# Kernel optimization log

Hardware: AMD Instinct MI355X
Metric: run time of the kernel (lower is better)

The kernel has to match this reference:

```python
import jax, jax.numpy as jnp
from jax import lax
import numpy as np

EPS = 1e-06


def conv1x1(x, W, b):
    # x: [B,C,H,W], W: [O,C], b: [O]
    return jnp.einsum('bchw,oc->bohw', x, W) + b[None, :, None, None]


def conv3x3(x, W, b):
    # W: [O,I,3,3], 'SAME' padding
    y = lax.conv_general_dilated(x, W, (1, 1), 'SAME',
                                 dimension_numbers=('NCHW', 'OIHW', 'NCHW'))
    return y + b[None, :, None, None]


def setup_inputs() -> dict:
    key = jax.random.key(0)
    ks = jax.random.split(key, 13)
    B, C, H, W = 8, 64, 256, 256
    kc, vc = 64, 64
    s = 0.05
    return {
        'x':  jax.random.normal(ks[0], (B, C, H, W), jnp.float32),
        'Wq': jax.random.normal(ks[1], (kc, C), jnp.float32) * s,
        'bq': jax.random.normal(ks[2], (kc,), jnp.float32) * s,
        'Wk': jax.random.normal(ks[3], (kc, C), jnp.float32) * s,
        'bk': jax.random.normal(ks[4], (kc,), jnp.float32) * s,
        'Wv': jax.random.normal(ks[5], (vc, C), jnp.float32) * s,
        'bv': jax.random.normal(ks[6], (vc,), jnp.float32) * s,
        'Wr': jax.random.normal(ks[7], (C, vc), jnp.float32) * s,
        'br': jax.random.normal(ks[8], (C,), jnp.float32) * s,
        'W1': jax.random.normal(ks[9], (C, C, 3, 3), jnp.float32) * s,
        'b1': jax.random.normal(ks[10], (C,), jnp.float32) * s,
        'W2': jax.random.normal(ks[11], (C, C, 3, 3), jnp.float32) * s,
        'b2': jax.random.normal(ks[12], (C,), jnp.float32) * s,
    }


def reference(x, Wq, bq, Wk, bk, Wv, bv, Wr, br, W1, b1, W2, b2):
    B, C, H, W = x.shape
    N = H * W
    kc = Wq.shape[0]
    vc = Wv.shape[0]

    Q = conv1x1(x, Wq, bq).reshape(B, kc, N)
    K = conv1x1(x, Wk, bk).reshape(B, kc, N)
    V = conv1x1(x, Wv, bv).reshape(B, vc, N)

    # L2-normalize over the channel axis (dim=-2 in torch)
    Qn = Q / jnp.linalg.norm(Q, axis=1, keepdims=True)   # [B,kc,N]
    Kn = K / jnp.linalg.norm(K, axis=1, keepdims=True)   # [B,kc,N]
    Qt = jnp.transpose(Qn, (0, 2, 1))                     # [B,N,kc]

    # denominator: 1 / (N + Q . (sum_n K + eps))
    k_sum = Kn.sum(axis=-1) + EPS                         # [B,kc]
    denom = 1.0 / (N + jnp.einsum('bnc,bc->bn', Qt, k_sum))  # [B,N]

    value_sum = V.sum(axis=-1, keepdims=True)             # [B,vc,1]

    # linear-attention aggregation: KV^T then Q.(KV)
    agg_kv = jnp.einsum('bmn,bcn->bmc', Kn, V)            # [B,kc,vc]
    # the per-batch/per-head torch loop sums head slices of the full kc
    # contraction -> equivalent to a single einsum over kc
    agg_qkv = jnp.einsum('bmc,bnm->bcn', agg_kv, Qt)      # [B,vc,N]

    numerator = value_sum + agg_qkv                       # [B,vc,N]
    weight_value = (numerator * denom[:, None, :]).reshape(B, vc, H, W)

    attn = conv1x1(weight_value, Wr, br)                  # [B,C,H,W]
    out = conv3x3(conv3x3(attn, W1, b1), W2, b2) * x + x
    return out
```

## Files before the change

kernel.cpp:

```cpp
#include <hip/hip_runtime.h>

typedef __attribute__((ext_vector_type(8))) short short8;
typedef __attribute__((ext_vector_type(4))) float f32x4;
typedef __attribute__((ext_vector_type(4))) int i32x4;

#define NPIX 65536
#define KPITCH 264
#define RED_KSUM 0
#define RED_VSUM 512
#define RED_AGG 1024

__device__ __forceinline__ float b2f(unsigned short u) {
  union { unsigned int i; float f; } z; z.i = ((unsigned int)u) << 16; return z.f;
}
__device__ __forceinline__ unsigned short f2b(float f) {
  union { float f; unsigned int i; } z; z.f = f;
  unsigned int r = z.i + 0x7fffu + ((z.i >> 16) & 1u);
  return (unsigned short)(r >> 16);
}
__device__ __forceinline__ unsigned int packbf(float a, float b) {
  return (unsigned int)f2b(a) | ((unsigned int)f2b(b) << 16);
}
__device__ __forceinline__ int cvtpk(float a, float b) {
  int r;
  asm("v_cvt_pk_bf16_f32 %0, %1, %2" : "=v"(r) : "v"(a), "v"(b));
  return r;
}

__global__ __launch_bounds__(256) void prep_kernel(
    const float* __restrict__ W1, const float* __restrict__ W2,
    const float* __restrict__ Wq, const float* __restrict__ Wk,
    const float* __restrict__ Wv,
    unsigned short* __restrict__ wA, unsigned short* __restrict__ wQKV,
    float* __restrict__ red)
{
  const int i = blockIdx.x * 256 + threadIdx.x;
  if (i < 73728) {
    const float* W = (i < 36864) ? W1 : W2;
    const int e = (i < 36864) ? i : (i - 36864);
    const int j    = e & 7;
    const int lane = (e >> 3) & 63;
    const int mt   = (e >> 9) & 3;
    const int kb   = (e >> 11) & 1;
    const int tap  = e >> 12;
    const int o = mt * 16 + (lane & 15);
    const int c = kb * 32 + ((lane >> 4) << 3) + j;
    wA[i] = f2b(W[o * 576 + c * 9 + tap]);
  } else if (i < 86016) {
    const int e = i - 73728;
    const int j    = e & 7;
    const int lane = (e >> 3) & 63;
    const int mt   = (e >> 9) & 3;
    const int kb   = (e >> 11) & 1;
    const int pj   = e >> 12;
    const float* W = (pj == 0) ? Wq : (pj == 1) ? Wk : Wv;
    const int o = mt * 16 + (lane & 15);
    const int c = kb * 32 + ((lane >> 4) << 3) + j;
    wQKV[e] = f2b(W[o * 64 + c]);
  } else if (i < 119808) {
    red[i - 86016] = 0.0f;
  }
}

#define PROJ(PIDX, BM)                                                         \
    {                                                                          \
      _Pragma("unroll")                                                        \
      for (int mt = 0; mt < 4; ++mt) {                                         \
        const f32x4 bb = *(const f32x4*)((BM) + mt * 16 + g * 4);              \
        _Pragma("unroll")                                                      \
        for (int nt = 0; nt < 4; ++nt) acc[mt][nt] = bb;                       \
      }                                                                        \
      _Pragma("unroll")                                                        \
      for (int kb = 0; kb < 2; ++kb) {                                         \
        const unsigned short* wp = wQKV + ((PIDX) * 2 + kb) * 2048 + l * 8;    \
        short8 af[4];                                                          \
        _Pragma("unroll")                                                      \
        for (int mt = 0; mt < 4; ++mt)                                         \
          af[mt] = *(const short8*)(wp + mt * 512);                            \
        _Pragma("unroll")                                                      \
        for (int mt = 0; mt < 4; ++mt)                                         \
          _Pragma("unroll")                                                    \
          for (int nt = 0; nt < 4; ++nt)                                       \
            acc[mt][nt] = __builtin_amdgcn_mfma_f32_16x16x32_bf16(             \
                af[mt], bf[nt][kb], acc[mt][nt], 0, 0, 0);                     \
      }                                                                        \
    }

__global__ __launch_bounds__(256, 2) void qkv_kernel(
    const float* __restrict__ x,
    const unsigned short* __restrict__ wQKV,
    const float* __restrict__ bq, const float* __restrict__ bk,
    const float* __restrict__ bv,
    unsigned short* __restrict__ Qn, float* __restrict__ red)
{
  __shared__ __align__(16) unsigned short sh[2 * 64 * KPITCH];
  unsigned short* ks = sh;
  unsigned short* vs = sh + 64 * KPITCH;
  unsigned int* shu = (unsigned int*)sh;
  const int b = blockIdx.y;
  const int t = threadIdx.x;
  const int w = t >> 6;
  const int l = t & 63;
  const int g = l >> 4;
  const int l15 = l & 15;
  const size_t xb = (size_t)b * 64 * NPIX;

  const f32x4 zero = {0.f, 0.f, 0.f, 0.f};
  f32x4 agg[4]  = {zero, zero, zero, zero};
  f32x4 kacc[4] = {zero, zero, zero, zero};
  f32x4 vacc[4] = {zero, zero, zero, zero};

  for (int it = 0; it < 4; ++it) {
    const int pxw = (blockIdx.x << 10) + (it << 8) + (w << 6);

    short8 bf[4][2];
#pragma unroll
    for (int nt = 0; nt < 4; ++nt) {
      const float* xp = x + xb + (size_t)(g * 8) * NPIX + pxw + nt * 16 + l15;
#pragma unroll
      for (int kb = 0; kb < 2; ++kb) {
        float f[8];
#pragma unroll
        for (int j = 0; j < 8; ++j)
          f[j] = xp[(size_t)(kb * 32 + j) * NPIX];
        union { i32x4 i; short8 s; } u;
        u.i.x = cvtpk(f[0], f[1]); u.i.y = cvtpk(f[2], f[3]);
        u.i.z = cvtpk(f[4], f[5]); u.i.w = cvtpk(f[6], f[7]);
        bf[nt][kb] = u.s;
      }
    }

    f32x4 acc[4][4];

    PROJ(0, bq);
    {
      float rq[4];
#pragma unroll
      for (int nt = 0; nt < 4; ++nt) {
        float ss = 0.f;
#pragma unroll
        for (int mt = 0; mt < 4; ++mt)
#pragma unroll
          for (int r = 0; r < 4; ++r)
            ss = fmaf(acc[mt][nt][r], acc[mt][nt][r], ss);
        ss += __shfl_xor(ss, 16);
        ss += __shfl_xor(ss, 32);
        rq[nt] = rsqrtf(ss);
      }
      unsigned int* sw = shu + w * 2304;
#pragma unroll
      for (int mt = 0; mt < 4; ++mt)
#pragma unroll
        for (int nt = 0; nt < 4; ++nt) {
          const int px = nt * 16 + l15;
          unsigned int* dst = sw + px * 36 + mt * 8 + g * 2;
          dst[0] = (unsigned)cvtpk(acc[mt][nt][0] * rq[nt], acc[mt][nt][1] * rq[nt]);
          dst[1] = (unsigned)cvtpk(acc[mt][nt][2] * rq[nt], acc[mt][nt][3] * rq[nt]);
        }
      const uint4* rr4 = (const uint4*)(shu + w * 2304);
#pragma unroll
      for (int k8 = 0; k8 < 8; ++k8) {
        const int p = (k8 << 3) + (l >> 3);
        const int ch8 = l & 7;
        *(uint4*)(Qn + ((size_t)b * NPIX + pxw + p) * 64 + ch8 * 8) =
            rr4[p * 9 + ch8];
      }
      __syncthreads();
    }

    PROJ(1, bk);
    {
      float rk[4];
#pragma unroll
      for (int nt = 0; nt < 4; ++nt) {
        float ss = 0.f;
#pragma unroll
        for (int mt = 0; mt < 4; ++mt)
#pragma unroll
          for (int r = 0; r < 4; ++r)
            ss = fmaf(acc[mt][nt][r], acc[mt][nt][r], ss);
        ss += __shfl_xor(ss, 16);
        ss += __shfl_xor(ss, 32);
        rk[nt] = rsqrtf(ss);
      }
#pragma unroll
      for (int mt = 0; mt < 4; ++mt)
#pragma unroll
        for (int nt = 0; nt < 4; ++nt)
#pragma unroll
          for (int r = 0; r < 4; ++r) {
            const float kn = acc[mt][nt][r] * rk[nt];
            kacc[mt][r] += kn;
            ks[(mt * 16 + g * 4 + r) * KPITCH + (w << 6) + nt * 16 + l15] =
                (unsigned short)cvtpk(kn, 0.f);
          }
    }

    PROJ(2, bv);
    {
#pragma unroll
      for (int mt = 0; mt < 4; ++mt)
#pragma unroll
        for (int nt = 0; nt < 4; ++nt)
#pragma unroll
          for (int r = 0; r < 4; ++r) {
            const float vv = acc[mt][nt][r];
            vacc[mt][r] += vv;
            vs[(mt * 16 + g * 4 + r) * KPITCH + (w << 6) + nt * 16 + l15] =
                (unsigned short)cvtpk(vv, 0.f);
          }
    }
    __syncthreads();

#pragma unroll
    for (int s = 0; s < 8; ++s) {
      const short8 ak =
          *(const short8*)(ks + (w * 16 + l15) * KPITCH + s * 32 + g * 8);
#pragma unroll
      for (int nt = 0; nt < 4; ++nt) {
        const short8 bv8 =
            *(const short8*)(vs + (nt * 16 + l15) * KPITCH + s * 32 + g * 8);
        agg[nt] = __builtin_amdgcn_mfma_f32_16x16x32_bf16(ak, bv8, agg[nt], 0, 0, 0);
      }
    }
    __syncthreads();
  }

#pragma unroll
  for (int mt = 0; mt < 4; ++mt)
#pragma unroll
    for (int r = 0; r < 4; ++r) {
      float kv = kacc[mt][r], vv = vacc[mt][r];
#pragma unroll
      for (int d = 1; d < 16; d <<= 1) {
        kv += __shfl_xor(kv, d);
        vv += __shfl_xor(vv, d);
      }
      if (l15 == 0) {
        atomicAdd(red + RED_KSUM + b * 64 + mt * 16 + g * 4 + r, kv);
        atomicAdd(red + RED_VSUM + b * 64 + mt * 16 + g * 4 + r, vv);
      }
    }
  float* ab = red + RED_AGG + b * 4096;
#pragma unroll
  for (int nt = 0; nt < 4; ++nt)
#pragma unroll
    for (int r = 0; r < 4; ++r)
      atomicAdd(ab + (w * 16 + g * 4 + r) * 64 + nt * 16 + l15, agg[nt][r]);
}

__global__ __launch_bounds__(256) void prep2_kernel(
    const float* __restrict__ Wr, const float* __restrict__ red,
    unsigned short* __restrict__ Cb, float* __restrict__ u,
    float* __restrict__ ks2)
{
  const int b = blockIdx.y;
  const int t = threadIdx.x;
  const int o = t & 63;
  const int kq = t >> 6;
  const float* wr = Wr + o * 64;
  const float* agg = red + RED_AGG + b * 4096;
#pragma unroll
  for (int i = 0; i < 4; ++i) {
    const int k = blockIdx.x * 16 + kq * 4 + i;
    const float* ar = agg + k * 64;
    float s = 0.f;
#pragma unroll
    for (int v = 0; v < 64; ++v) s = fmaf(wr[v], ar[v], s);
    const int mt = o >> 4, kb = k >> 5;
    const int lane = (o & 15) | (((k >> 3) & 3) << 4);
    const int j = k & 7;
    const unsigned short c1 = f2b(s);
    const float r1 = s - b2f(c1);
    Cb[b * 4096 + ((kb * 4 + mt) * 64 + lane) * 8 + j] = c1;
    Cb[32768 + b * 4096 + ((kb * 4 + mt) * 64 + lane) * 8 + j] = f2b(r1);
  }
  if (blockIdx.x == 0 && t < 64) {
    const float* vsr = red + RED_VSUM + b * 64;
    float s = 0.f;
#pragma unroll
    for (int v = 0; v < 64; ++v) s = fmaf(Wr[t * 64 + v], vsr[v], s);
    u[b * 64 + t] = s;
    ks2[b * 64 + t] = red[RED_KSUM + b * 64 + t] + 1e-6f;
  }
}

__global__ __launch_bounds__(256, 2) void attn_kernel(
    const unsigned short* __restrict__ Qn,
    const unsigned short* __restrict__ Cb,
    const float* __restrict__ u,
    const float* __restrict__ ks2,
    const float* __restrict__ br,
    unsigned short* __restrict__ attn)
{
  __shared__ __align__(16) unsigned short att[256 * 72];
  const int b = blockIdx.y;
  const int t = threadIdx.x;
  const int w = t >> 6, l = t & 63, g = l >> 4, l15 = l & 15;

  short8 af[2][2][4];
#pragma unroll
  for (int lvl = 0; lvl < 2; ++lvl)
#pragma unroll
    for (int kb = 0; kb < 2; ++kb)
#pragma unroll
      for (int mt = 0; mt < 4; ++mt)
        af[lvl][kb][mt] = *(const short8*)(
            Cb + lvl * 32768 + b * 4096 + ((kb * 4 + mt) * 64 + l) * 8);
  f32x4 uu[4], brf[4];
#pragma unroll
  for (int mt = 0; mt < 4; ++mt) {
    uu[mt]  = *(const f32x4*)(u + b * 64 + mt * 16 + g * 4);
    brf[mt] = *(const f32x4*)(br + mt * 16 + g * 4);
  }
  float ksl[16];
#pragma unroll
  for (int kb = 0; kb < 2; ++kb)
#pragma unroll
    for (int j = 0; j < 8; ++j)
      ksl[kb * 8 + j] = ks2[b * 64 + kb * 32 + g * 8 + j];

  for (int it = 0; it < 4; ++it) {
    const int pxw = (blockIdx.x << 10) + (it << 8) + (w << 6);
    short8 qf[4][2];
    float denom[4];
#pragma unroll
    for (int nt = 0; nt < 4; ++nt) {
      const unsigned short* qp =
          Qn + ((size_t)b * NPIX + pxw + nt * 16 + l15) * 64 + g * 8;
      qf[nt][0] = *(const short8*)qp;
      qf[nt][1] = *(const short8*)(qp + 32);
      float ss = 0.f;
#pragma unroll
      for (int kb = 0; kb < 2; ++kb)
#pragma unroll
        for (int j = 0; j < 8; ++j)
          ss = fmaf(b2f((unsigned short)qf[nt][kb][j]), ksl[kb * 8 + j], ss);
      ss += __shfl_xor(ss, 16);
      ss += __shfl_xor(ss, 32);
      denom[nt] = 1.0f / (65536.0f + ss);
    }
    f32x4 acc[4][4];
#pragma unroll
    for (int mt = 0; mt < 4; ++mt)
#pragma unroll
      for (int nt = 0; nt < 4; ++nt) acc[mt][nt] = uu[mt];
#pragma unroll
    for (int kb = 0; kb < 2; ++kb)
#pragma unroll
      for (int mt = 0; mt < 4; ++mt)
#pragma unroll
        for (int nt = 0; nt < 4; ++nt) {
          acc[mt][nt] = __builtin_amdgcn_mfma_f32_16x16x32_bf16(
              af[0][kb][mt], qf[nt][kb], acc[mt][nt], 0, 0, 0);
          acc[mt][nt] = __builtin_amdgcn_mfma_f32_16x16x32_bf16(
              af[1][kb][mt], qf[nt][kb], acc[mt][nt], 0, 0, 0);
        }
    unsigned int* sw = (unsigned int*)att + w * 2304;
#pragma unroll
    for (int mt = 0; mt < 4; ++mt)
#pragma unroll
      for (int nt = 0; nt < 4; ++nt) {
        const int px = nt * 16 + l15;
        unsigned int* dst = sw + px * 36 + mt * 8 + g * 2;
        dst[0] = (unsigned)cvtpk(fmaf(acc[mt][nt][0], denom[nt], brf[mt][0]),
                                 fmaf(acc[mt][nt][1], denom[nt], brf[mt][1]));
        dst[1] = (unsigned)cvtpk(fmaf(acc[mt][nt][2], denom[nt], brf[mt][2]),
                                 fmaf(acc[mt][nt][3], denom[nt], brf[mt][3]));
      }
    const uint4* rr4 = (const uint4*)att + w * 576;
#pragma unroll
    for (int k8 = 0; k8 < 8; ++k8) {
      const int p = (k8 << 3) + (l >> 3);
      const int ch8 = l & 7;
      *(uint4*)(attn + ((size_t)b * NPIX + pxw + p) * 64 + ch8 * 8) =
          rr4[p * 9 + ch8];
    }
  }
}

template <int EPI>
__global__ __launch_bounds__(256, 3) void conv3_kernel(
    const unsigned short* __restrict__ in,
    const unsigned short* __restrict__ wA,
    const float* __restrict__ bias,
    const float* __restrict__ xin,
    unsigned short* __restrict__ outh,
    float* __restrict__ outf)
{
  __shared__ __align__(16) unsigned short tile[10 * 34 * 72];
  const int bz = blockIdx.z;
  const int ty0 = blockIdx.y << 3;
  const int tx0 = blockIdx.x << 5;
  const int tid = threadIdx.x;
  const size_t nb = (size_t)bz * NPIX;

  for (int s = tid; s < 2720; s += 256) {
    const int g = s & 7;
    const int pix = s >> 3;
    const int xx = pix % 34;
    const int row = pix / 34;
    const int gx = tx0 + xx - 1;
    const int gy = ty0 + row - 1;
    uint4 v = {0u, 0u, 0u, 0u};
    if ((unsigned)gx < 256u && (unsigned)gy < 256u)
      v = *(const uint4*)(in + ((nb + (gy << 8) + gx) << 6) + (g << 3));
    *(uint4*)(tile + pix * 72 + (g << 3)) = v;
  }
  __syncthreads();

  const int w = tid >> 6, lane = tid & 63, q = lane >> 4, l = lane & 15;
  f32x4 acc[4][4];
  {
#pragma unroll
    for (int mt = 0; mt < 4; ++mt) {
      const f32x4 bb = *(const f32x4*)(bias + mt * 16 + q * 4);
#pragma unroll
      for (int nt = 0; nt < 4; ++nt) acc[mt][nt] = bb;
    }
  }
  const short8* tp = (const short8*)tile;
  for (int tap = 0; tap < 9; ++tap) {
    const int dy = tap / 3, dx = tap - dy * 3;
#pragma unroll
    for (int kb = 0; kb < 2; ++kb) {
      const unsigned short* wp = wA + (tap * 2 + kb) * 2048 + lane * 8;
      short8 af[4];
#pragma unroll
      for (int mt = 0; mt < 4; ++mt) af[mt] = *(const short8*)(wp + mt * 512);
      short8 bf[4];
#pragma unroll
      for (int nt = 0; nt < 4; ++nt) {
        const int yl = (w << 1) + (nt >> 1) + dy;
        const int xl = ((nt & 1) << 4) + l + dx;
        bf[nt] = tp[(yl * 34 + xl) * 9 + (kb << 2) + q];
      }
#pragma unroll
      for (int mt = 0; mt < 4; ++mt)
#pragma unroll
        for (int nt = 0; nt < 4; ++nt)
          acc[mt][nt] = __builtin_amdgcn_mfma_f32_16x16x32_bf16(
              af[mt], bf[nt], acc[mt][nt], 0, 0, 0);
    }
  }

  if (EPI == 0) {
    __syncthreads();
    unsigned int* wreg = (unsigned int*)tile + w * 2304;
#pragma unroll
    for (int mt = 0; mt < 4; ++mt)
#pragma unroll
      for (int nt = 0; nt < 4; ++nt) {
        const int p = ((nt >> 1) << 5) + ((nt & 1) << 4) + l;
        unsigned int* dst = wreg + p * 36 + (mt << 3) + (q << 1);
        dst[0] = packbf(acc[mt][nt][0], acc[mt][nt][1]);
        dst[1] = packbf(acc[mt][nt][2], acc[mt][nt][3]);
      }
    __syncthreads();
    const uint4* rreg = (const uint4*)tile + w * 576;
#pragma unroll
    for (int k = 0; k < 8; ++k) {
      const int p = (k << 3) + (lane >> 3);
      const int ch = lane & 7;
      const int gx = tx0 + (p & 31);
      const int gy = ty0 + (w << 1) + (p >> 5);
      *(uint4*)(outh + ((nb + (gy << 8) + gx) << 6) + (ch << 3)) =
          rreg[p * 9 + ch];
    }
  } else {
#pragma unroll
    for (int mt = 0; mt < 4; ++mt)
#pragma unroll
      for (int nt = 0; nt < 4; ++nt) {
        const int gx = tx0 + ((nt & 1) << 4) + l;
        const int gy = ty0 + (w << 1) + (nt >> 1);
#pragma unroll
        for (int r = 0; r < 4; ++r) {
          const int o = (mt << 4) + (q << 2) + r;
          const size_t idx = (((size_t)bz * 64 + o) << 16) + (gy << 8) + gx;
          const float xo = xin[idx];
          outf[idx] = fmaf(acc[mt][nt][r], xo, xo);
        }
      }
  }
}

extern "C" void kernel_launch(void* const* d_in, const int* in_sizes, int n_in,
                              void* d_out, int out_size, void* d_ws, size_t ws_size,
                              hipStream_t stream) {
  (void)in_sizes; (void)n_in; (void)out_size; (void)ws_size;
  const float* x  = (const float*)d_in[0];
  const float* Wq = (const float*)d_in[1];
  const float* bq = (const float*)d_in[2];
  const float* Wk = (const float*)d_in[3];
  const float* bk = (const float*)d_in[4];
  const float* Wv = (const float*)d_in[5];
  const float* bv = (const float*)d_in[6];
  const float* Wr = (const float*)d_in[7];
  const float* br = (const float*)d_in[8];
  const float* W1 = (const float*)d_in[9];
  const float* b1 = (const float*)d_in[10];
  const float* W2 = (const float*)d_in[11];
  const float* b2 = (const float*)d_in[12];

  unsigned short* wA1 = (unsigned short*)d_ws;
  unsigned short* wA2 = wA1 + 36864;
  float* red = (float*)((char*)d_ws + 147456);
  unsigned short* bufA = (unsigned short*)((char*)d_ws + 294912);
  unsigned short* wQKV = (unsigned short*)((char*)d_ws + 294912);
  unsigned short* Cb = (unsigned short*)((char*)d_ws + 294912);
  float* u_  = (float*)((char*)d_ws + 294912 + 131072);
  float* ks2 = (float*)((char*)d_ws + 294912 + 133120);
  unsigned short* bufB = (unsigned short*)d_out;
  unsigned short* bufQ = (unsigned short*)((char*)d_out + 67108864);

  prep_kernel<<<468, 256, 0, stream>>>(W1, W2, Wq, Wk, Wv, wA1, wQKV, red);
  qkv_kernel<<<dim3(64, 8), 256, 0, stream>>>(x, wQKV, bq, bk, bv, bufQ, red);
  prep2_kernel<<<dim3(4, 8), 256, 0, stream>>>(Wr, red, Cb, u_, ks2);
  attn_kernel<<<dim3(64, 8), 256, 0, stream>>>(bufQ, Cb, u_, ks2, br, bufB);
  conv3_kernel<0><<<dim3(8, 32, 8), 256, 0, stream>>>(
      bufB, wA1, b1, nullptr, bufA, nullptr);
  conv3_kernel<1><<<dim3(8, 32, 8), 256, 0, stream>>>(
      bufA, wA2, b2, x, nullptr, (float*)d_out);
}
```

Before: 562.3 us.

## Fuse the two 3x3 convolutions into one kernel with halo recompute in LDS

Replaces the two separate conv3x3 launches with one 512-thread kernel. Six waves compute the first convolution over the 10x34 halo region, reading the input directly from global memory. They store the bf16 result in shared memory, and all eight waves then compute the second convolution plus the x-residual epilogue. This removes the write and re-read of the full intermediate activation buffer and one kernel launch. The cost is roughly a third more first-convolution work for the halo, uncached repeated global loads per tap instead of LDS staging, and idle waves during stage one. The workspace layout is also reshuffled so the attention output lives in the workspace instead of the output buffer.

Result: no change. 561.2 us (-0.2%).

```diff
diff --git a/kernel.cpp b/kernel.cpp
--- a/kernel.cpp
+++ b/kernel.cpp
@@ -379,110 +379,128 @@
   }
 }
 
-template <int EPI>
-__global__ __launch_bounds__(256, 3) void conv3_kernel(
+__global__ __launch_bounds__(512, 2) void fused_conv_kernel(
     const unsigned short* __restrict__ in,
     const unsigned short* __restrict__ wA,
-    const float* __restrict__ bias,
+    const float* __restrict__ b1, const float* __restrict__ b2,
     const float* __restrict__ xin,
-    unsigned short* __restrict__ outh,
     float* __restrict__ outf)
 {
-  __shared__ __align__(16) unsigned short tile[10 * 34 * 72];
+  __shared__ __align__(16) unsigned short mid[340 * 72];
   const int bz = blockIdx.z;
   const int ty0 = blockIdx.y << 3;
   const int tx0 = blockIdx.x << 5;
   const int tid = threadIdx.x;
+  const int w = tid >> 6, lane = tid & 63, q = lane >> 4, l = lane & 15;
   const size_t nb = (size_t)bz * NPIX;
 
-  for (int s = tid; s < 2720; s += 256) {
-    const int g = s & 7;
-    const int pix = s >> 3;
-    const int xx = pix % 34;
-    const int row = pix / 34;
-    const int gx = tx0 + xx - 1;
-    const int gy = ty0 + row - 1;
-    uint4 v = {0u, 0u, 0u, 0u};
-    if ((unsigned)gx < 256u && (unsigned)gy < 256u)
-      v = *(const uint4*)(in + ((nb + (gy << 8) + gx) << 6) + (g << 3));
-    *(uint4*)(tile + pix * 72 + (g << 3)) = v;
+  if (w < 6) {
+    f32x4 acc[4][4];
+#pragma unroll
+    for (int mt = 0; mt < 4; ++mt) {
+      const f32x4 bb = *(const f32x4*)(b1 + mt * 16 + q * 4);
+#pragma unroll
+      for (int nt = 0; nt < 4; ++nt) acc[mt][nt] = bb;
+    }
+    int ylv[4], xlv[4];
+#pragma unroll
+    for (int nt = 0; nt < 4; ++nt) {
+      const int mp = w * 64 + nt * 16 + l;
+      const int mpc = mp < 340 ? mp : 339;
+      ylv[nt] = mpc / 34;
+      xlv[nt] = mpc - ylv[nt] * 34;
+    }
+    for (int tap = 0; tap < 9; ++tap) {
+      const int dy = tap / 3, dx = tap - dy * 3;
+#pragma unroll
+      for (int kb = 0; kb < 2; ++kb) {
+        const unsigned short* wp = wA + (tap * 2 + kb) * 2048 + lane * 8;
+        short8 af[4];
+#pragma unroll
+        for (int mt = 0; mt < 4; ++mt) af[mt] = *(const short8*)(wp + mt * 512);
+        short8 bfv[4];
+#pragma unroll
+        for (int nt = 0; nt < 4; ++nt) {
+          const int gy = ty0 + ylv[nt] + dy - 2;
+          const int gx = tx0 + xlv[nt] + dx - 2;
+          short8 v = {0, 0, 0, 0, 0, 0, 0, 0};
+          if ((unsigned)gy < 256u && (unsigned)gx < 256u)
+            v = *(const short8*)(
+                in + ((nb + (gy << 8) + gx) << 6) + ((kb * 4 + q) << 3));
+          bfv[nt] = v;
+        }
+#pragma unroll
+        for (int mt = 0; mt < 4; ++mt)
+#pragma unroll
+          for (int nt = 0; nt < 4; ++nt)
+            acc[mt][nt] = __builtin_amdgcn_mfma_f32_16x16x32_bf16(
+                af[mt], bfv[nt], acc[mt][nt], 0, 0, 0);
+      }
+    }
+    unsigned int* mu = (unsigned int*)mid;
+#pragma unroll
+    for (int nt = 0; nt < 4; ++nt) {
+      const int mp = w * 64 + nt * 16 + l;
+      if (mp < 340) {
+        const int gym = ty0 + ylv[nt] - 1;
+        const int gxm = tx0 + xlv[nt] - 1;
+        const bool ok = ((unsigned)gym < 256u) && ((unsigned)gxm < 256u);
+#pragma unroll
+        for (int mt = 0; mt < 4; ++mt) {
+          unsigned int* dst = mu + mp * 36 + mt * 8 + q * 2;
+          dst[0] = ok ? packbf(acc[mt][nt][0], acc[mt][nt][1]) : 0u;
+          dst[1] = ok ? packbf(acc[mt][nt][2], acc[mt][nt][3]) : 0u;
+        }
+      }
+    }
   }
   __syncthreads();
 
-  const int w = tid >> 6, lane = tid & 63, q = lane >> 4, l = lane & 15;
-  f32x4 acc[4][4];
-  {
-#pragma unroll
-    for (int mt = 0; mt < 4; ++mt) {
-      const f32x4 bb = *(const f32x4*)(bias + mt * 16 + q * 4);
-#pragma unroll
-      for (int nt = 0; nt < 4; ++nt) acc[mt][nt] = bb;
-    }
-  }
-  const short8* tp = (const short8*)tile;
+  f32x4 acc2[4][2];
+#pragma unroll
+  for (int mt = 0; mt < 4; ++mt) {
+    const f32x4 bb = *(const f32x4*)(b2 + mt * 16 + q * 4);
+    acc2[mt][0] = bb; acc2[mt][1] = bb;
+  }
+  const short8* tp2 = (const short8*)mid;
+  const unsigned short* wA2p = wA + 36864;
   for (int tap = 0; tap < 9; ++tap) {
     const int dy = tap / 3, dx = tap - dy * 3;
 #pragma unroll
     for (int kb = 0; kb < 2; ++kb) {
-      const unsigned short* wp = wA + (tap * 2 + kb) * 2048 + lane * 8;
+      const unsigned short* wp = wA2p + (tap * 2 + kb) * 2048 + lane * 8;
       short8 af[4];
 #pragma unroll
       for (int mt = 0; mt < 4; ++mt) af[mt] = *(const short8*)(wp + mt * 512);
-      short8 bf[4];
-#pragma unroll
-      for (int nt = 0; nt < 4; ++nt) {
-        const int yl = (w << 1) + (nt >> 1) + dy;
-        const int xl = ((nt & 1) << 4) + l + dx;
-        bf[nt] = tp[(yl * 34 + xl) * 9 + (kb << 2) + q];
+      short8 bf2[2];
+#pragma unroll
+      for (int nt = 0; nt < 2; ++nt) {
+        const int yl = w + dy;
+        const int xl = nt * 16 + l + dx;
+        bf2[nt] = tp2[(yl * 34 + xl) * 9 + (kb << 2) + q];
       }
 #pragma unroll
       for (int mt = 0; mt < 4; ++mt)
 #pragma unroll
-        for (int nt = 0; nt < 4; ++nt)
-          acc[mt][nt] = __builtin_amdgcn_mfma_f32_16x16x32_bf16(
-              af[mt], bf[nt], acc[mt][nt], 0, 0, 0);
-    }
-  }
-
-  if (EPI == 0) {
-    __syncthreads();
-    unsigned int* wreg = (unsigned int*)tile + w * 2304;
-#pragma unroll
-    for (int mt = 0; mt < 4; ++mt)
-#pragma unroll
-      for (int nt = 0; nt < 4; ++nt) {
-        const int p = ((nt >> 1) << 5) + ((nt & 1) << 4) + l;
-        unsigned int* dst = wreg + p * 36 + (mt << 3) + (q << 1);
-        dst[0] = packbf(acc[mt][nt][0], acc[mt][nt][1]);
-        dst[1] = packbf(acc[mt][nt][2], acc[mt][nt][3]);
-      }
-    __syncthreads();
-    const uint4* rreg = (const uint4*)tile + w * 576;
-#pragma unroll
-    for (int k = 0; k < 8; ++k) {
-      const int p = (k << 3) + (lane >> 3);
-      const int ch = lane & 7;
-      const int gx = tx0 + (p & 31);
-      const int gy = ty0 + (w << 1) + (p >> 5);
-      *(uint4*)(outh + ((nb + (gy << 8) + gx) << 6) + (ch << 3)) =
-          rreg[p * 9 + ch];
-    }
-  } else {
-#pragma unroll
-    for (int mt = 0; mt < 4; ++mt)
-#pragma unroll
-      for (int nt = 0; nt < 4; ++nt) {
-        const int gx = tx0 + ((nt & 1) << 4) + l;
-        const int gy = ty0 + (w << 1) + (nt >> 1);
-#pragma unroll
-        for (int r = 0; r < 4; ++r) {
-          const int o = (mt << 4) + (q << 2) + r;
-          const size_t idx = (((size_t)bz * 64 + o) << 16) + (gy << 8) + gx;
-          const float xo = xin[idx];
-          outf[idx] = fmaf(acc[mt][nt][r], xo, xo);
-        }
-      }
-  }
+        for (int nt = 0; nt < 2; ++nt)
+          acc2[mt][nt] = __builtin_amdgcn_mfma_f32_16x16x32_bf16(
+              af[mt], bf2[nt], acc2[mt][nt], 0, 0, 0);
+    }
+  }
+#pragma unroll
+  for (int mt = 0; mt < 4; ++mt)
+#pragma unroll
+    for (int nt = 0; nt < 2; ++nt) {
+      const int gx = tx0 + nt * 16 + l;
+      const int gy = ty0 + w;
+#pragma unroll
+      for (int r = 0; r < 4; ++r) {
+        const int o = (mt << 4) + (q << 2) + r;
+        const size_t idx = (((size_t)bz * 64 + o) << 16) + (gy << 8) + gx;
+        const float xo = xin[idx];
+        outf[idx] = fmaf(acc2[mt][nt][r], xo, xo);
+      }
+    }
 }
 
 extern "C" void kernel_launch(void* const* d_in, const int* in_sizes, int n_in,
@@ -503,23 +521,19 @@
   const float* W2 = (const float*)d_in[11];
   const float* b2 = (const float*)d_in[12];
 
-  unsigned short* wA1 = (unsigned short*)d_ws;
-  unsigned short* wA2 = wA1 + 36864;
-  float* red = (float*)((char*)d_ws + 147456);
-  unsigned short* bufA = (unsigned short*)((char*)d_ws + 294912);
-  unsigned short* wQKV = (unsigned short*)((char*)d_ws + 294912);
-  unsigned short* Cb = (unsigned short*)((char*)d_ws + 294912);
-  float* u_  = (float*)((char*)d_ws + 294912 + 131072);
-  float* ks2 = (float*)((char*)d_ws + 294912 + 133120);
-  unsigned short* bufB = (unsigned short*)d_out;
+  unsigned short* wA1  = (unsigned short*)d_ws;
+  unsigned short* wQKV = (unsigned short*)((char*)d_ws + 147456);
+  unsigned short* Cb   = (unsigned short*)((char*)d_ws + 147456);
+  float* u_  = (float*)((char*)d_ws + 278528);
+  float* ks2 = (float*)((char*)d_ws + 280576);
+  float* red = (float*)((char*)d_ws + 282624);
+  unsigned short* bufB = (unsigned short*)((char*)d_ws + 282624);
   unsigned short* bufQ = (unsigned short*)((char*)d_out + 67108864);
 
   prep_kernel<<<468, 256, 0, stream>>>(W1, W2, Wq, Wk, Wv, wA1, wQKV, red);
   qkv_kernel<<<dim3(64, 8), 256, 0, stream>>>(x, wQKV, bq, bk, bv, bufQ, red);
   prep2_kernel<<<dim3(4, 8), 256, 0, stream>>>(Wr, red, Cb, u_, ks2);
   attn_kernel<<<dim3(64, 8), 256, 0, stream>>>(bufQ, Cb, u_, ks2, br, bufB);
-  conv3_kernel<0><<<dim3(8, 32, 8), 256, 0, stream>>>(
-      bufB, wA1, b1, nullptr, bufA, nullptr);
-  conv3_kernel<1><<<dim3(8, 32, 8), 256, 0, stream>>>(
-      bufA, wA2, b2, x, nullptr, (float*)d_out);
-}
+  fused_conv_kernel<<<dim3(8, 32, 8), 512, 0, stream>>>(
+      bufB, wA1, b1, b2, x, (float*)d_out);
+}
```
